# Kernel tuning notes

Hardware: AMD Instinct MI355X
Metric: run time of the kernel (lower is better)

## Reference

```python
import jax, jax.numpy as jnp
import numpy as np

N, E = 50000, 640000
D_IN, D_OUT, N_BASES = 128, 128, 8


def setup_inputs() -> dict:
    key = jax.random.key(0)
    k1, k2, k3, k4, k5, k6 = jax.random.split(key, 6)
    x = jax.random.normal(k1, (N, D_IN), dtype=jnp.float32)
    edge_index = jax.random.randint(k2, (2, E), 0, N, dtype=jnp.int64)
    # basis-decomposed relation weights (num_relations=1)
    bases = jax.random.normal(k3, (N_BASES, D_IN, D_OUT), dtype=jnp.float32) * 0.05
    comp = jax.random.normal(k4, (1, N_BASES), dtype=jnp.float32)
    root = jax.random.normal(k5, (D_IN, D_OUT), dtype=jnp.float32) * 0.05
    bias = jax.random.normal(k6, (D_OUT,), dtype=jnp.float32) * 0.01
    return {"x": x, "edge_index": edge_index, "bases": bases,
            "comp": comp, "root": root, "bias": bias}


def reference(x, edge_index, bases, comp, root, bias):
    # W[rel=0] = sum_b comp[0,b] * bases[b]  -> [D_IN, D_OUT]
    W = jnp.einsum('b,bio->io', comp[0], bases)
    src = edge_index[0]  # message sources (x_j)
    dst = edge_index[1]  # aggregation targets
    # gather -> scatter-add (aggr='add'), then relation-specific transform
    agg = jax.ops.segment_sum(x[src], dst, num_segments=x.shape[0])  # [N, D_IN]
    out = agg @ W + x @ root + bias  # root/self-loop transform + bias
    return out
```

## Files before the change

### kernel.cpp

```cpp
#include <hip/hip_runtime.h>

#define N_NODES 50000
#define N_EDGES 640000
#define D 128
#define NB 8
#define PAD 32
#define NSTRIP 3125

#define BUCKET_B 256
#define GEMM_B   1536

typedef _Float16 half_t;
typedef __attribute__((ext_vector_type(8))) _Float16 half8;
typedef __attribute__((ext_vector_type(4))) float f32x4;

__global__ __launch_bounds__(256)
void init_kernel(const float* __restrict__ bases,
                 const float* __restrict__ comp,
                 const float* __restrict__ root,
                 half_t* __restrict__ Wt,
                 half_t* __restrict__ Rt,
                 half_t* __restrict__ y,
                 int* __restrict__ cnt,
                 int* __restrict__ novf) {
    int i = blockIdx.x * 256 + threadIdx.x;
    if (i == 0) *novf = 0;
    if (i < N_NODES) cnt[i] = 0;
    if (i < D) y[(size_t)N_NODES * D + i] = (half_t)0.f;
    if (i < D * D) {
        int ii = i >> 7, o = i & 127;
        float acc = 0.f;
#pragma unroll
        for (int b = 0; b < NB; ++b)
            acc += comp[b] * bases[((size_t)b * D + ii) * D + o];
        Wt[o * D + ii] = (half_t)acc;
        Rt[o * D + ii] = (half_t)root[i];
    }
}

__global__ __launch_bounds__(256, 4)
void fused_kernel(const float* __restrict__ x,
                  const half_t* __restrict__ Wt,
                  const half_t* __restrict__ Rt,
                  const float* __restrict__ bias,
                  const int* __restrict__ eidx,
                  half_t* __restrict__ y,
                  float* __restrict__ out,
                  int* __restrict__ cnt,
                  int* __restrict__ bucket,
                  int* __restrict__ ovf,
                  int* __restrict__ novf) {
    const int tid = threadIdx.x;

    if (blockIdx.x < BUCKET_B) {
        int t = blockIdx.x * 256 + tid;
        for (int e = t; e < N_EDGES; e += BUCKET_B * 256) {
            int src = eidx[e];
            int dst = eidx[N_EDGES + e];
            int pos = atomicAdd(&cnt[dst], 1);
            if (pos < PAD) {
                bucket[(size_t)dst * PAD + pos] = src;
            } else {
                int k = atomicAdd(novf, 1);
                ovf[2 * k]     = src;
                ovf[2 * k + 1] = dst;
            }
        }
        return;
    }

    __shared__ half_t ldsY[16 * 136];
    __shared__ float  ldsO[16 * 132];

    const int gb   = blockIdx.x - BUCKET_B;
    const int wave = tid >> 6;
    const int lane = tid & 63;
    const int m    = lane & 15;
    const int quad = lane >> 4;
    const int q    = wave;

    half8 bw[2][4], br[2][4];
    float bb[2];
#pragma unroll
    for (int t = 0; t < 2; ++t) {
        const int nt = 2 * q + t;
        const half_t* wp = Wt + (nt * 16 + m) * D + quad * 8;
        const half_t* rp = Rt + (nt * 16 + m) * D + quad * 8;
#pragma unroll
        for (int kk = 0; kk < 4; ++kk) {
            bw[t][kk] = *(const half8*)(wp + kk * 32);
            br[t][kk] = *(const half8*)(rp + kk * 32);
        }
        bb[t] = bias[nt * 16 + m];
    }

    const float4* x4 = (const float4*)x;
    const int row_o = tid >> 4, cq = tid & 15;

    for (int s = gb; s < NSTRIP; s += GEMM_B) {
        size_t ab = (size_t)(s * 16 + m) * 32 + quad * 2;
        half8 a[4];
#pragma unroll
        for (int kk = 0; kk < 4; ++kk) {
            float4 v0 = x4[ab + kk * 8];
            float4 v1 = x4[ab + kk * 8 + 1];
            half8 h;
            h[0] = (half_t)v0.x; h[1] = (half_t)v0.y; h[2] = (half_t)v0.z; h[3] = (half_t)v0.w;
            h[4] = (half_t)v1.x; h[5] = (half_t)v1.y; h[6] = (half_t)v1.z; h[7] = (half_t)v1.w;
            a[kk] = h;
        }

        f32x4 accW[2], accR[2];
#pragma unroll
        for (int t = 0; t < 2; ++t) {
            accW[t] = (f32x4){0.f, 0.f, 0.f, 0.f};
            accR[t] = (f32x4){0.f, 0.f, 0.f, 0.f};
        }
#pragma unroll
        for (int t = 0; t < 2; ++t)
#pragma unroll
            for (int kk = 0; kk < 4; ++kk) {
                accW[t] = __builtin_amdgcn_mfma_f32_16x16x32_f16(a[kk], bw[t][kk], accW[t], 0, 0, 0);
                accR[t] = __builtin_amdgcn_mfma_f32_16x16x32_f16(a[kk], br[t][kk], accR[t], 0, 0, 0);
            }

#pragma unroll
        for (int t = 0; t < 2; ++t) {
            const int nt = 2 * q + t;
#pragma unroll
            for (int r = 0; r < 4; ++r) {
                ldsY[(quad * 4 + r) * 136 + nt * 16 + m] = (half_t)accW[t][r];
                ldsO[(quad * 4 + r) * 132 + nt * 16 + m] = accR[t][r] + bb[t];
            }
        }
        __syncthreads();

        {
            half8 hy = *(const half8*)(ldsY + row_o * 136 + cq * 8);
            *(half8*)(y + (size_t)(s * 16 + row_o) * D + cq * 8) = hy;
            const float* so = ldsO + row_o * 132 + cq * 8;
            float4 o0 = *(const float4*)(so);
            float4 o1 = *(const float4*)(so + 4);
            float4* op = (float4*)(out + (size_t)(s * 16 + row_o) * D + cq * 8);
            op[0] = o0;
            op[1] = o1;
        }
        __syncthreads();
    }
}

__global__ __launch_bounds__(256)
void gather_kernel(const int* __restrict__ cnt,
                   const int* __restrict__ bucket,
                   const half_t* __restrict__ y,
                   const int* __restrict__ ovf,
                   const int* __restrict__ novf,
                   float* __restrict__ out) {
    const int wave = threadIdx.x >> 6;
    const int lane = threadIdx.x & 63;
    const int g    = lane >> 4;
    const int q    = lane & 15;
    const int node = blockIdx.x * 4 + wave;
    if (node >= N_NODES) return;

    int c_raw = cnt[node];
    int c = c_raw > PAD ? PAD : c_raw;
    const int* bp = bucket + (size_t)node * PAD;

    int base = (c * g) >> 2;
    int ng   = ((c * (g + 1)) >> 2) - base;

    int idx[8];
#pragma unroll
    for (int j = 0; j < 8; ++j)
        idx[j] = (j < ng) ? bp[base + j] : N_NODES;

    half8 v[8];
#pragma unroll
    for (int j = 0; j < 8; ++j)
        v[j] = *(const half8*)(y + (size_t)idx[j] * D + q * 8);

    float acc[8];
#pragma unroll
    for (int t = 0; t < 8; ++t)
        acc[t] = (((float)v[0][t] + (float)v[1][t]) + ((float)v[2][t] + (float)v[3][t]))
               + (((float)v[4][t] + (float)v[5][t]) + ((float)v[6][t] + (float)v[7][t]));

    if (c_raw > PAD) {
        int n = *novf;
        for (int k = g; k < n; k += 4) {
            if (ovf[2 * k + 1] == node) {
                half8 w = *(const half8*)(y + (size_t)ovf[2 * k] * D + q * 8);
#pragma unroll
                for (int t = 0; t < 8; ++t) acc[t] += (float)w[t];
            }
        }
    }

#pragma unroll
    for (int t = 0; t < 8; ++t) {
        acc[t] += __shfl_xor(acc[t], 16);
        acc[t] += __shfl_xor(acc[t], 32);
    }

    if (g == 0) {
        float4* op = (float4*)(out + (size_t)node * D + q * 8);
        float4 o0 = op[0], o1 = op[1];
        o0.x += acc[0]; o0.y += acc[1]; o0.z += acc[2]; o0.w += acc[3];
        o1.x += acc[4]; o1.y += acc[5]; o1.z += acc[6]; o1.w += acc[7];
        op[0] = o0; op[1] = o1;
    }
}

extern "C" void kernel_launch(void* const* d_in, const int* in_sizes, int n_in,
                              void* d_out, int out_size, void* d_ws, size_t ws_size,
                              hipStream_t stream) {
    const float* x     = (const float*)d_in[0];
    const int*   eidx  = (const int*)d_in[1];
    const float* bases = (const float*)d_in[2];
    const float* comp  = (const float*)d_in[3];
    const float* root  = (const float*)d_in[4];
    const float* bias  = (const float*)d_in[5];
    float* out = (float*)d_out;

    char* ws = (char*)d_ws;
    half_t* y      = (half_t*)ws;
    half_t* Wt     = (half_t*)(ws + 12800512);
    half_t* Rt     = (half_t*)(ws + 12833280);
    int*    cnt    = (int*)   (ws + 12866048);
    int*    bucket = (int*)   (ws + 13066048);
    int*    novf   = (int*)   (ws + 19466048);
    int*    ovf    = (int*)   (ws + 19466064);

    init_kernel<<<(N_NODES + 255) / 256, 256, 0, stream>>>(
        bases, comp, root, Wt, Rt, y, cnt, novf);
    fused_kernel<<<BUCKET_B + GEMM_B, 256, 0, stream>>>(
        x, Wt, Rt, bias, eidx, y, out, cnt, bucket, ovf, novf);
    gather_kernel<<<(N_NODES + 3) / 4, 256, 0, stream>>>(
        cnt, bucket, y, ovf, novf, out);
}
```

Baseline: 157.2 us.

## Move root transform and bias into gather kernel, drop out round-trip

Only the x@W product stays in the fused kernel, and its output now goes straight to y with scattered 2-byte stores instead of LDS staging. The gather kernel now computes x@root+bias per 16-node strip with MFMA into LDS, then adds the aggregated neighbour sum and writes out once. This removes the write and re-read of the intermediate out buffer and halves the GEMM work in the first kernel, which also gets fewer GEMM blocks. The risks are uncoalesced half-precision stores to y and re-reading x in the gather kernel. Neighbour index loads are also changed to a fixed 8 per quad instead of a split over the count.

```diff
diff --git a/kernel.cpp b/kernel.cpp
--- a/kernel.cpp
+++ b/kernel.cpp
@@ -6,9 +6,10 @@
 #define NB 8
 #define PAD 32
 #define NSTRIP 3125
+#define NBLK_G 3125
 
 #define BUCKET_B 256
-#define GEMM_B   1536
+#define GEMM_B   768
 
 typedef _Float16 half_t;
 typedef __attribute__((ext_vector_type(8))) _Float16 half8;
@@ -41,11 +42,8 @@
 __global__ __launch_bounds__(256, 4)
 void fused_kernel(const float* __restrict__ x,
                   const half_t* __restrict__ Wt,
-                  const half_t* __restrict__ Rt,
-                  const float* __restrict__ bias,
                   const int* __restrict__ eidx,
                   half_t* __restrict__ y,
-                  float* __restrict__ out,
                   int* __restrict__ cnt,
                   int* __restrict__ bucket,
                   int* __restrict__ ovf,
@@ -69,9 +67,6 @@
         return;
     }
 
-    __shared__ half_t ldsY[16 * 136];
-    __shared__ float  ldsO[16 * 132];
-
     const int gb   = blockIdx.x - BUCKET_B;
     const int wave = tid >> 6;
     const int lane = tid & 63;
@@ -79,24 +74,16 @@
     const int quad = lane >> 4;
     const int q    = wave;
 
-    half8 bw[2][4], br[2][4];
-    float bb[2];
+    half8 bw[2][4];
 #pragma unroll
     for (int t = 0; t < 2; ++t) {
-        const int nt = 2 * q + t;
-        const half_t* wp = Wt + (nt * 16 + m) * D + quad * 8;
-        const half_t* rp = Rt + (nt * 16 + m) * D + quad * 8;
-#pragma unroll
-        for (int kk = 0; kk < 4; ++kk) {
+        const half_t* wp = Wt + ((2 * q + t) * 16 + m) * D + quad * 8;
+#pragma unroll
+        for (int kk = 0; kk < 4; ++kk)
             bw[t][kk] = *(const half8*)(wp + kk * 32);
-            br[t][kk] = *(const half8*)(rp + kk * 32);
-        }
-        bb[t] = bias[nt * 16 + m];
     }
 
     const float4* x4 = (const float4*)x;
-    const int row_o = tid >> 4, cq = tid & 15;
-
     for (int s = gb; s < NSTRIP; s += GEMM_B) {
         size_t ab = (size_t)(s * 16 + m) * 32 + quad * 2;
         half8 a[4];
@@ -110,105 +97,142 @@
             a[kk] = h;
         }
 
-        f32x4 accW[2], accR[2];
+        f32x4 accW[2];
+#pragma unroll
+        for (int t = 0; t < 2; ++t) accW[t] = (f32x4){0.f, 0.f, 0.f, 0.f};
+#pragma unroll
+        for (int t = 0; t < 2; ++t)
+#pragma unroll
+            for (int kk = 0; kk < 4; ++kk)
+                accW[t] = __builtin_amdgcn_mfma_f32_16x16x32_f16(a[kk], bw[t][kk], accW[t], 0, 0, 0);
+
 #pragma unroll
         for (int t = 0; t < 2; ++t) {
-            accW[t] = (f32x4){0.f, 0.f, 0.f, 0.f};
-            accR[t] = (f32x4){0.f, 0.f, 0.f, 0.f};
-        }
-#pragma unroll
-        for (int t = 0; t < 2; ++t)
-#pragma unroll
-            for (int kk = 0; kk < 4; ++kk) {
-                accW[t] = __builtin_amdgcn_mfma_f32_16x16x32_f16(a[kk], bw[t][kk], accW[t], 0, 0, 0);
-                accR[t] = __builtin_amdgcn_mfma_f32_16x16x32_f16(a[kk], br[t][kk], accR[t], 0, 0, 0);
-            }
-
-#pragma unroll
-        for (int t = 0; t < 2; ++t) {
-            const int nt = 2 * q + t;
-#pragma unroll
-            for (int r = 0; r < 4; ++r) {
-                ldsY[(quad * 4 + r) * 136 + nt * 16 + m] = (half_t)accW[t][r];
-                ldsO[(quad * 4 + r) * 132 + nt * 16 + m] = accR[t][r] + bb[t];
-            }
-        }
-        __syncthreads();
-
-        {
-            half8 hy = *(const half8*)(ldsY + row_o * 136 + cq * 8);
-            *(half8*)(y + (size_t)(s * 16 + row_o) * D + cq * 8) = hy;
-            const float* so = ldsO + row_o * 132 + cq * 8;
-            float4 o0 = *(const float4*)(so);
-            float4 o1 = *(const float4*)(so + 4);
-            float4* op = (float4*)(out + (size_t)(s * 16 + row_o) * D + cq * 8);
-            op[0] = o0;
-            op[1] = o1;
-        }
-        __syncthreads();
+            int col = (2 * q + t) * 16 + m;
+#pragma unroll
+            for (int r = 0; r < 4; ++r)
+                y[(size_t)(s * 16 + quad * 4 + r) * D + col] = (half_t)accW[t][r];
+        }
     }
 }
 
 __global__ __launch_bounds__(256)
-void gather_kernel(const int* __restrict__ cnt,
+void gather_kernel(const float* __restrict__ x,
+                   const half_t* __restrict__ Rt,
+                   const float* __restrict__ bias,
+                   const int* __restrict__ cnt,
                    const int* __restrict__ bucket,
                    const half_t* __restrict__ y,
                    const int* __restrict__ ovf,
                    const int* __restrict__ novf,
                    float* __restrict__ out) {
-    const int wave = threadIdx.x >> 6;
-    const int lane = threadIdx.x & 63;
-    const int g    = lane >> 4;
-    const int q    = lane & 15;
-    const int node = blockIdx.x * 4 + wave;
-    if (node >= N_NODES) return;
-
-    int c_raw = cnt[node];
-    int c = c_raw > PAD ? PAD : c_raw;
-    const int* bp = bucket + (size_t)node * PAD;
-
-    int base = (c * g) >> 2;
-    int ng   = ((c * (g + 1)) >> 2) - base;
-
-    int idx[8];
-#pragma unroll
-    for (int j = 0; j < 8; ++j)
-        idx[j] = (j < ng) ? bp[base + j] : N_NODES;
-
-    half8 v[8];
-#pragma unroll
-    for (int j = 0; j < 8; ++j)
-        v[j] = *(const half8*)(y + (size_t)idx[j] * D + q * 8);
-
-    float acc[8];
-#pragma unroll
-    for (int t = 0; t < 8; ++t)
-        acc[t] = (((float)v[0][t] + (float)v[1][t]) + ((float)v[2][t] + (float)v[3][t]))
-               + (((float)v[4][t] + (float)v[5][t]) + ((float)v[6][t] + (float)v[7][t]));
-
-    if (c_raw > PAD) {
-        int n = *novf;
-        for (int k = g; k < n; k += 4) {
-            if (ovf[2 * k + 1] == node) {
-                half8 w = *(const half8*)(y + (size_t)ovf[2 * k] * D + q * 8);
-#pragma unroll
-                for (int t = 0; t < 8; ++t) acc[t] += (float)w[t];
+    __shared__ float ldsO[16 * 132];
+
+    const int tid  = threadIdx.x;
+    const int wave = tid >> 6;
+    const int lane = tid & 63;
+    const int m    = lane & 15;
+    const int quad = lane >> 4;
+    const int nb   = blockIdx.x;
+
+    {
+        half8 br[2][4];
+        float bb[2];
+#pragma unroll
+        for (int t = 0; t < 2; ++t) {
+            const int nt = 2 * wave + t;
+            const half_t* rp = Rt + (nt * 16 + m) * D + quad * 8;
+#pragma unroll
+            for (int kk = 0; kk < 4; ++kk)
+                br[t][kk] = *(const half8*)(rp + kk * 32);
+            bb[t] = bias[nt * 16 + m];
+        }
+
+        const float4* x4 = (const float4*)x;
+        size_t ab = (size_t)(nb * 16 + m) * 32 + quad * 2;
+        half8 a[4];
+#pragma unroll
+        for (int kk = 0; kk < 4; ++kk) {
+            float4 v0 = x4[ab + kk * 8];
+            float4 v1 = x4[ab + kk * 8 + 1];
+            half8 h;
+            h[0] = (half_t)v0.x; h[1] = (half_t)v0.y; h[2] = (half_t)v0.z; h[3] = (half_t)v0.w;
+            h[4] = (half_t)v1.x; h[5] = (half_t)v1.y; h[6] = (half_t)v1.z; h[7] = (half_t)v1.w;
+            a[kk] = h;
+        }
+
+        f32x4 accR[2];
+#pragma unroll
+        for (int t = 0; t < 2; ++t) accR[t] = (f32x4){0.f, 0.f, 0.f, 0.f};
+#pragma unroll
+        for (int t = 0; t < 2; ++t)
+#pragma unroll
+            for (int kk = 0; kk < 4; ++kk)
+                accR[t] = __builtin_amdgcn_mfma_f32_16x16x32_f16(a[kk], br[t][kk], accR[t], 0, 0, 0);
+
+#pragma unroll
+        for (int t = 0; t < 2; ++t) {
+            const int nt = 2 * wave + t;
+#pragma unroll
+            for (int r = 0; r < 4; ++r)
+                ldsO[(quad * 4 + r) * 132 + nt * 16 + m] = accR[t][r] + bb[t];
+        }
+    }
+    __syncthreads();
+
+    for (int i = 0; i < 4; ++i) {
+        const int node = nb * 16 + wave * 4 + i;
+        const int* bp = bucket + (size_t)node * PAD;
+
+        int c_raw = cnt[node];
+        int idx[8];
+#pragma unroll
+        for (int j = 0; j < 8; ++j)
+            idx[j] = bp[quad * 8 + j];
+
+        int c = c_raw > PAD ? PAD : c_raw;
+#pragma unroll
+        for (int j = 0; j < 8; ++j)
+            idx[j] = (quad * 8 + j < c) ? idx[j] : N_NODES;
+
+        half8 v[8];
+#pragma unroll
+        for (int j = 0; j < 8; ++j)
+            v[j] = *(const half8*)(y + (size_t)idx[j] * D + m * 8);
+
+        float acc[8];
+#pragma unroll
+        for (int t = 0; t < 8; ++t)
+            acc[t] = (((float)v[0][t] + (float)v[1][t]) + ((float)v[2][t] + (float)v[3][t]))
+                   + (((float)v[4][t] + (float)v[5][t]) + ((float)v[6][t] + (float)v[7][t]));
+
+        if (c_raw > PAD) {
+            int n = *novf;
+            for (int k = quad; k < n; k += 4) {
+                if (ovf[2 * k + 1] == node) {
+                    half8 w = *(const half8*)(y + (size_t)ovf[2 * k] * D + m * 8);
+#pragma unroll
+                    for (int t = 0; t < 8; ++t) acc[t] += (float)w[t];
+                }
             }
         }
-    }
-
-#pragma unroll
-    for (int t = 0; t < 8; ++t) {
-        acc[t] += __shfl_xor(acc[t], 16);
-        acc[t] += __shfl_xor(acc[t], 32);
-    }
-
-    if (g == 0) {
-        float4* op = (float4*)(out + (size_t)node * D + q * 8);
-        float4 o0 = op[0], o1 = op[1];
-        o0.x += acc[0]; o0.y += acc[1]; o0.z += acc[2]; o0.w += acc[3];
-        o1.x += acc[4]; o1.y += acc[5]; o1.z += acc[6]; o1.w += acc[7];
-        op[0] = o0; op[1] = o1;
+
+#pragma unroll
+        for (int t = 0; t < 8; ++t) {
+            acc[t] += __shfl_xor(acc[t], 16);
+            acc[t] += __shfl_xor(acc[t], 32);
+        }
+
+        if (quad == 0) {
+            const float* so = ldsO + (wave * 4 + i) * 132 + m * 8;
+            float4 o0 = *(const float4*)(so);
+            float4 o1 = *(const float4*)(so + 4);
+            o0.x += acc[0]; o0.y += acc[1]; o0.z += acc[2]; o0.w += acc[3];
+            o1.x += acc[4]; o1.y += acc[5]; o1.z += acc[6]; o1.w += acc[7];
+            float4* op = (float4*)(out + (size_t)node * D + m * 8);
+            op[0] = o0;
+            op[1] = o1;
+        }
     }
 }
 
@@ -235,7 +259,7 @@
     init_kernel<<<(N_NODES + 255) / 256, 256, 0, stream>>>(
         bases, comp, root, Wt, Rt, y, cnt, novf);
     fused_kernel<<<BUCKET_B + GEMM_B, 256, 0, stream>>>(
-        x, Wt, Rt, bias, eidx, y, out, cnt, bucket, ovf, novf);
-    gather_kernel<<<(N_NODES + 3) / 4, 256, 0, stream>>>(
-        cnt, bucket, y, ovf, novf, out);
-}
+        x, Wt, eidx, y, cnt, bucket, ovf, novf);
+    gather_kernel<<<NBLK_G, 256, 0, stream>>>(
+        x, Rt, bias, cnt, bucket, y, ovf, novf, out);
+}
```

Result: slower. 167.6 us (+6.6%).
